# Performance work log

Measured on AMD Instinct MI355X. Metric: run time of the kernel, lower is better.

## Reference

```python
import jax, jax.numpy as jnp
import numpy as np

B, S, F, I, E, TOP_K, K, D, CLASSES = 2, 2048, 512, 1024, 8, 2, 7, 2, 8192
BETA = 0.9
INIT_SCALE = D ** -0.5


def setup_inputs() -> dict:
    key = jax.random.key(0)
    ks = jax.random.split(key, 10)
    s = lambda *shape: shape
    return {
        "inp": jax.random.randint(ks[0], (B, S), 0, CLASSES),
        "embed": jax.random.normal(ks[1], (CLASSES, 2 * F), jnp.float32) * 0.02,
        "gate_in_w": jax.random.normal(ks[2], (D, F, E), jnp.float32) * (F ** -0.5),
        "w_in": jax.random.normal(ks[3], (D, E, F, I), jnp.float32) * (F ** -0.5),
        "conv_w": jax.random.normal(ks[4], (D, I, I, K), jnp.float32) * ((I * K) ** -0.5),
        "gate_out_w": jax.random.normal(ks[5], (D, I, E), jnp.float32) * (I ** -0.5),
        "w_out": jax.random.normal(ks[6], (D, E, I, 3 * F), jnp.float32) * (I ** -0.5),
        "out_w": jax.random.normal(ks[7], (CLASSES, 2 * F), jnp.float32) * ((2 * F) ** -0.5),
        "out_b": jnp.zeros((CLASSES,), jnp.float32),
    }


def _moe(x, gate_w, expert_w):
    # x: [T, Fin]; NaiveGate top-k routing + grouped-GEMM combine.
    logits = x @ gate_w                                  # [T, E]
    top_vals, top_idx = jax.lax.top_k(logits, TOP_K)     # [T, k]
    scores = jax.nn.softmax(top_vals, axis=-1)           # softmax over selected experts
    n_exp = gate_w.shape[1]
    combine = jnp.sum(scores[:, :, None] * jax.nn.one_hot(top_idx, n_exp, dtype=x.dtype), axis=1)  # [T, E]
    y = jnp.einsum("tf,efo->teo", x, expert_w)           # dense all-expert eval
    return jnp.einsum("teo,te->to", y, combine)


def _norm(out):
    # custom norm over channel dim (dim 1 of [B, C, S])
    out = out - out.mean(axis=1, keepdims=True)
    c = out.shape[1]
    return out / (jnp.linalg.norm(out, axis=1, keepdims=True) * (c ** -0.5) + 1e-5)


def _cell(x, gate_in, win, cw, gate_out, wout, divisor):
    # x: [B, F, S]
    b, f, seq = x.shape
    t = x.transpose(0, 2, 1).reshape(b * seq, f)
    h = jax.nn.relu(_moe(t, gate_in, win))               # [T, I]
    h = h.reshape(b, seq, -1).transpose(0, 2, 1)         # [B, I, S]
    # causal depthwise-style conv (groups=1), left-pad K-1
    h = jax.lax.conv_general_dilated(h, cw, (1,), [(cw.shape[-1] - 1, 0)],
                                     dimension_numbers=("NCH", "OIH", "NCH"))
    h = jax.nn.relu(h)
    t2 = h.transpose(0, 2, 1).reshape(b * seq, -1)
    o = _moe(t2, gate_out, wout).reshape(b, seq, 3 * f).transpose(0, 2, 1)  # [B, 3F, S]
    depth_, scale, shift = jnp.split(o, 3, axis=1)
    cum = jnp.cumsum(depth_, axis=2)                      # running sum over sequence
    out = cum / divisor * scale + shift
    return _norm(out) * INIT_SCALE


def reference(inp, embed, gate_in_w, w_in, conv_w, gate_out_w, w_out, out_w, out_b):
    emb = embed[inp]                                      # [B, S, 2F]
    x = emb.transpose(0, 2, 1)                            # [B, 2F, S]
    x0, x1 = x[:, :F], x[:, F:]
    divisor = (jnp.arange(S, dtype=x.dtype) + 1.0)[None, None, :]
    for d in range(D):
        # momentum coupling with LinearAttentionCell
        f = _cell(x1, gate_in_w[d], w_in[d], conv_w[d], gate_out_w[d], w_out[d], divisor)
        y = x0 * BETA + f * (1.0 - BETA)
        x0, x1 = x1, y
        # additive coupling with Identity
        y = x0 + x1
        x0, x1 = x1, y
    out = jnp.concatenate([x0, x1], axis=1)               # [B, 2F, S]
    logits = jnp.einsum("bcs,kc->bks", out, out_w) + out_b[None, :, None]
    return logits
```

## Files before the change

### kernel.cpp

```cpp
#include <hip/hip_runtime.h>
#include <math.h>

typedef unsigned short u16;
typedef unsigned int   u32;

#define B_ 2
#define S_ 2048
#define F_ 512
#define I_ 1024
#define E_ 8
#define KW_ 7
#define D_ 2
#define CLASSES_ 8192
#define T_ (B_*S_)
#define SP_ (S_+6)
#define NSLOT_ 9216
#define GMAX_ 72

typedef __bf16 bf16x8 __attribute__((ext_vector_type(8)));
typedef float  f32x4  __attribute__((ext_vector_type(4)));

__device__ __forceinline__ u16 f2b(float f) {
    u32 x = __float_as_uint(f);
    return (u16)((x + 0x7fffu + ((x >> 16) & 1u)) >> 16);
}
__device__ __forceinline__ void fsplit(float v, u16& h, u16& l) {
    u16 hh = f2b(v);
    float hv = __uint_as_float(((u32)hh) << 16);
    h = hh;
    l = f2b(v - hv);
}

template<int N> __device__ __forceinline__ void waitvm() {
    asm volatile("s_waitcnt vmcnt(%0)" :: "n"(N) : "memory");
}

#define GLDS16(g, l) __builtin_amdgcn_global_load_lds( \
    (const __attribute__((address_space(1))) u32*)(g), \
    (__attribute__((address_space(3))) u32*)(l), 16, 0, 0)

__global__ void embed_k(const int* __restrict__ inp, const float* __restrict__ emb,
                        float* __restrict__ X0, float* __restrict__ X1,
                        int* __restrict__ stok, int* __restrict__ cnt)
{
    int t = blockIdx.x;
    int r = inp[t];
    const float* e = emb + (size_t)r * (2*F_);
    for (int c = threadIdx.x; c < F_; c += 256) {
        X0[(size_t)t*F_ + c] = e[c];
        X1[(size_t)t*F_ + c] = e[F_ + c];
    }
    int gi = blockIdx.x * 256 + threadIdx.x;
    if (gi < NSLOT_) stok[gi] = -1;
    if (gi < E_) cnt[gi] = 0;
}

template<int MODE, int W>
__global__ __launch_bounds__(512) void gatev_k(const float* __restrict__ X,
                                               const float* __restrict__ X2,
                                               const float* __restrict__ GW,
                                               int2* __restrict__ e2, float2* __restrict__ w2,
                                               int* __restrict__ cnt)
{
    __shared__ float gw[W*E_];
    for (int i = threadIdx.x; i < W*E_; i += 512) {
        int f = i >> 3, e = i & 7;
        gw[e*W + f] = GW[i];
    }
    __syncthreads();
    int wv = threadIdx.x >> 6, l = threadIdx.x & 63;
    int t = blockIdx.x * 8 + wv;
    const float* xr  = X + (size_t)t * W;
    const float* x2r = MODE ? (X2 + (size_t)t * W) : nullptr;
    float a[8];
    #pragma unroll
    for (int e = 0; e < 8; e++) a[e] = 0.f;
    #pragma unroll
    for (int c = 0; c < W/256; c++) {
        int f = c*256 + l*4;
        float4 x = *(const float4*)(xr + f);
        if (MODE) {
            float4 y = *(const float4*)(x2r + f);
            x.x = fmaxf(x.x + y.x, 0.f); x.y = fmaxf(x.y + y.y, 0.f);
            x.z = fmaxf(x.z + y.z, 0.f); x.w = fmaxf(x.w + y.w, 0.f);
        }
        #pragma unroll
        for (int e = 0; e < 8; e++) {
            float4 g = *(const float4*)(gw + e*W + f);
            a[e] += x.x*g.x + x.y*g.y + x.z*g.z + x.w*g.w;
        }
    }
    #pragma unroll
    for (int e = 0; e < 8; e++) {
        #pragma unroll
        for (int off = 32; off; off >>= 1) a[e] += __shfl_xor(a[e], off);
    }
    if (l == 0) {
        float v0 = -3.4e38f, v1 = -3.4e38f; int i0 = 0, i1 = 0;
        #pragma unroll
        for (int k = 0; k < E_; k++) {
            float v = a[k];
            if (v > v0)      { v1 = v0; i1 = i0; v0 = v; i0 = k; }
            else if (v > v1) { v1 = v;  i1 = k; }
        }
        float ex = expf(v1 - v0);
        e2[t] = make_int2(i0, i1);
        w2[t] = make_float2(1.f/(1.f+ex), ex/(1.f+ex));
        atomicAdd(&cnt[i0], 1);
        atomicAdd(&cnt[i1], 1);
    }
}

__global__ __launch_bounds__(256) void schedscat_k(const int* __restrict__ cnt,
                                                   const int2* __restrict__ e2,
                                                   const float2* __restrict__ w2,
                                                   int4* __restrict__ s0, int4* __restrict__ s1,
                                                   int split,
                                                   int* __restrict__ stok, float* __restrict__ sw)
{
    __shared__ int lpos[E_];
    int tid = threadIdx.x;
    int nb[E_], slotst[E_], gst[E_];
    int poff = 0, g0 = 0, g1 = 0;
    #pragma unroll
    for (int e = 0; e < E_; e++) {
        int n = (cnt[e] + 127) >> 7;
        nb[e] = n;
        slotst[e] = poff;
        if (e < split) { gst[e] = g0; g0 += n; }
        else           { gst[e] = g1; g1 += n; }
        poff += n << 7;
    }
    if (tid < E_) lpos[tid] = slotst[tid];
    if (tid < GMAX_) {
        int4 en = make_int4(0,0,0,0);
        for (int e = 0; e < split; e++)
            if (tid >= gst[e] && tid < gst[e] + nb[e])
                en = make_int4(slotst[e] + (tid - gst[e])*128, e, 1, 0);
        s0[tid] = en;
    }
    if (split < E_ && tid >= 128 && tid < 128 + GMAX_) {
        int j = tid - 128;
        int4 en = make_int4(0,0,0,0);
        for (int e = split; e < E_; e++)
            if (j >= gst[e] && j < gst[e] + nb[e])
                en = make_int4(slotst[e] + (j - gst[e])*128, e - split, 1, 0);
        s1[j] = en;
    }
    __syncthreads();
    for (int t = tid; t < T_; t += 256) {
        int2 e = e2[t]; float2 w = w2[t];
        int p0 = atomicAdd(&lpos[e.x], 1);
        stok[p0] = t;          sw[p0] = w.x;
        int p1 = atomicAdd(&lpos[e.y], 1);
        stok[p1] = t | 4096;   sw[p1] = w.y;
    }
}

__global__ __launch_bounds__(256) void transp_k(const float* __restrict__ src0,
                                                u16* __restrict__ dh, u16* __restrict__ dl,
                                                int R, int C)
{
    __shared__ float tl[32][33];
    int z = blockIdx.z;
    const float* src = src0 + (size_t)z * R * C;
    size_t dbase = (size_t)z * R * C;
    int c0 = blockIdx.x * 32, r0 = blockIdx.y * 32;
    int tx = threadIdx.x & 31, ty = threadIdx.x >> 5;
    #pragma unroll
    for (int j = 0; j < 32; j += 8)
        tl[ty + j][tx] = src[(size_t)(r0 + ty + j) * C + c0 + tx];
    __syncthreads();
    #pragma unroll
    for (int j = 0; j < 32; j += 8) {
        u16 h, l; fsplit(tl[tx][ty + j], h, l);
        size_t idx = dbase + (size_t)(c0 + ty + j) * R + r0 + tx;
        dh[idx] = h; dl[idx] = l;
    }
}

__global__ __launch_bounds__(256) void convw_k(const float* __restrict__ src,
                                               u16* __restrict__ dh, u16* __restrict__ dl)
{
    __shared__ float row[KW_*I_];
    int o = blockIdx.x;
    const float* s = src + (size_t)o * (KW_*I_);
    for (int c = threadIdx.x; c < KW_*I_; c += 256) row[c] = s[c];
    __syncthreads();
    size_t base = (size_t)o * (KW_*I_);
    for (int j = threadIdx.x; j < KW_*I_; j += 256) {
        int kc = j >> 10, i = j & 1023;
        u16 h, l; fsplit(row[i*KW_ + kc], h, l);
        dh[base + j] = h; dl[base + j] = l;
    }
}

__global__ void split_k(const float* __restrict__ src, u16* __restrict__ dh, u16* __restrict__ dl)
{
    size_t i = ((size_t)blockIdx.x * 256 + threadIdx.x) * 4;
    float4 v = *(const float4*)(src + i);
    ushort4 oh, ol;
    fsplit(v.x, oh.x, ol.x); fsplit(v.y, oh.y, ol.y);
    fsplit(v.z, oh.z, ol.z); fsplit(v.w, oh.w, ol.w);
    *(ushort4*)(dh + i) = oh;
    *(ushort4*)(dl + i) = ol;
}

__global__ void splith_k(const float* __restrict__ src, u16* __restrict__ dh)
{
    size_t i = ((size_t)blockIdx.x * 256 + threadIdx.x) * 4;
    float4 v = *(const float4*)(src + i);
    ushort4 oh;
    oh.x = f2b(v.x); oh.y = f2b(v.y); oh.z = f2b(v.z); oh.w = f2b(v.w);
    *(ushort4*)(dh + i) = oh;
}

__global__ void hsplit_k(const float* __restrict__ Ha, const float* __restrict__ Hb,
                         u16* __restrict__ ph, u16* __restrict__ pl)
{
    int gid = blockIdx.x*256 + threadIdx.x;
    int eb = gid * 4;
    int t = eb >> 10, c = eb & 1023;
    float4 a = *(const float4*)(Ha + eb);
    float4 b = *(const float4*)(Hb + eb);
    ushort4 hh, ll;
    fsplit(fmaxf(a.x+b.x,0.f), hh.x, ll.x); fsplit(fmaxf(a.y+b.y,0.f), hh.y, ll.y);
    fsplit(fmaxf(a.z+b.z,0.f), hh.z, ll.z); fsplit(fmaxf(a.w+b.w,0.f), hh.w, ll.w);
    size_t row = (size_t)(t >> 11)*SP_ + 6 + (t & (S_-1));
    *(ushort4*)(ph + (row << 10) + c) = hh;
    *(ushort4*)(pl + (row << 10) + c) = ll;
}

__global__ void crelu_k(const float* __restrict__ a0, const float* __restrict__ a1,
                        u16* __restrict__ dh, u16* __restrict__ dl,
                        int* __restrict__ stok, int* __restrict__ cnt)
{
    size_t i = ((size_t)blockIdx.x * 256 + threadIdx.x) * 4;
    float4 a = *(const float4*)(a0 + i);
    float4 b = *(const float4*)(a1 + i);
    ushort4 hh, ll;
    fsplit(fmaxf(a.x+b.x,0.f), hh.x, ll.x); fsplit(fmaxf(a.y+b.y,0.f), hh.y, ll.y);
    fsplit(fmaxf(a.z+b.z,0.f), hh.z, ll.z); fsplit(fmaxf(a.w+b.w,0.f), hh.w, ll.w);
    *(ushort4*)(dh + i) = hh;
    *(ushort4*)(dl + i) = ll;
    int gi = blockIdx.x * 256 + threadIdx.x;
    if (gi < NSLOT_) stok[gi] = -1;
    if (gi < E_) cnt[gi] = 0;
}

__global__ void hpadzero_k(u16* __restrict__ ph, u16* __restrict__ pl)
{
    int idx = blockIdx.x*256 + threadIdx.x;
    int b = idx / (6*I_);
    int rem = idx - b*(6*I_);
    size_t a = ((size_t)b*SP_ + (rem >> 10))*I_ + (rem & 1023);
    ph[a] = 0; pl[a] = 0;
}

enum { A_SPLIT=0, A_CONV=1, A_GATHER2=2 };
enum { EP_RANK=0, EP_DUAL=1, EP_FINAL=2 };

#define SBSZ(Pv) ((((Pv)==3)?16384:8192) + 8192*(((Pv)>=2)?2:1))

template<int AM, int EP, int PASSES, int SWZ, int PRIO>
__global__ __launch_bounds__(256, ((2*SBSZ(PASSES)) <= 32768) ? 4 : (((2*SBSZ(PASSES)) <= 49152) ? 3 : 2))
void mgemm(const void* __restrict__ A1, const void* __restrict__ A2,
           const u16* __restrict__ Bh, const u16* __restrict__ Bl,
           float* __restrict__ Ca, float* __restrict__ Cb,
           int N, int Kd, int ldb,
           const int4* __restrict__ sched, const int* __restrict__ stok,
           const float* __restrict__ sw, const float* __restrict__ bias)
{
    constexpr bool HAL = (PASSES==3);
    constexpr bool HBL = (PASSES>=2);
    constexpr int OAL  = 8192;
    constexpr int OBH  = (HAL ? 16384 : 8192);
    constexpr int OBL  = OBH + 8192;
    constexpr int SB   = OBH + 8192*(HBL ? 2 : 1);
    constexpr int NLOADS = 2*(HBL ? 2 : 1) + 2*(HAL ? 2 : 1);
    __shared__ uint4 ldsv[2*SB/16];
    char* lds = (char*)ldsv;

    const int tid  = threadIdx.x;
    const int lane = tid & 63, wid = tid >> 6;
    int n0 = blockIdx.x * 128;

    int slot0 = 0, m0 = 0, koff = 0, kz = 0;
    const u16 *bhb = Bh, *blb = Bl;
    if (AM == A_GATHER2) {
        int4 sc = sched[blockIdx.y];
        if (!sc.z) return;
        slot0 = sc.x;
        size_t wo = (size_t)sc.y * N * ldb;
        bhb = Bh + wo; blb = Bl + wo;
    } else if (AM == A_CONV) {
        if (SWZ == 1) {
            int fid = blockIdx.y * 8 + blockIdx.x;
            int xcd = fid & 7, k = fid >> 3;
            int mp = (xcd >> 1) * 8 + (k >> 3);
            int np = (xcd & 1) * 8 + (k & 7);
            m0 = mp * 128;
            kz = np >> 3;
            koff = kz * Kd;
            n0 = (np & 7) * 128;
        } else {
            m0 = (blockIdx.y & 31) * 128;
            kz = blockIdx.y >> 5;
            koff = kz * Kd;
        }
    } else {
        m0 = blockIdx.y * 128;
    }

    int srow[2], klog[2];
    #pragma unroll
    for (int c = 0; c < 2; c++) {
        int row = (tid >> 2) + c*64;
        srow[c] = row;
        klog[c] = ((tid & 3) ^ ((row >> 1) & 3)) << 3;
    }

    const u16 *bgh[2], *bgl[2];
    #pragma unroll
    for (int c = 0; c < 2; c++) {
        size_t off = (size_t)(n0 + srow[c]) * ldb + koff + klog[c];
        bgh[c] = bhb + off;
        bgl[c] = blb + off;
    }

    const u16 *a1p[2], *a2p[2];
    #pragma unroll
    for (int c = 0; c < 2; c++) {
        if (AM == A_SPLIT) {
            size_t off = (size_t)(m0 + srow[c]) * Kd + klog[c];
            a1p[c] = (const u16*)A1 + off;
            a2p[c] = (const u16*)A2 + off;
        } else if (AM == A_CONV) {
            int t = m0 + srow[c];
            size_t rb = (((size_t)(t >> 11)*SP_ + (t & (S_-1))) << 10) + koff + klog[c];
            a1p[c] = (const u16*)A1 + rb;
            a2p[c] = (const u16*)A2 + rb;
        } else {
            int s = stok[slot0 + srow[c]];
            int tk = (s < 0) ? 0 : (s & 4095);
            size_t off = (size_t)tk * Kd + klog[c];
            a1p[c] = (const u16*)A1 + off;
            a2p[c] = (const u16*)A2 + off;
        }
    }

    const int wr = wid >> 1, wc = wid & 1;
    const int l15 = lane & 15, kq = lane >> 4;
    int aoff[4], boff[4];
    #pragma unroll
    for (int m = 0; m < 4; m++) {
        int ra = wr*64 + m*16 + l15;
        aoff[m] = ra*64 + ((kq ^ ((ra >> 1) & 3)) << 4);
    }
    #pragma unroll
    for (int n = 0; n < 4; n++) {
        int rb = wc*64 + n*16 + l15;
        boff[n] = rb*64 + ((kq ^ ((rb >> 1) & 3)) << 4);
    }

    f32x4 acc[4][4];
    #pragma unroll
    for (int m = 0; m < 4; m++)
        #pragma unroll
        for (int n = 0; n < 4; n++) acc[m][n] = {0.f,0.f,0.f,0.f};

    const int nt = Kd >> 5;

#define STAGE_GL(K0, BB)                                                          \
    {                                                                             \
        _Pragma("unroll")                                                         \
        for (int c = 0; c < 2; c++) {                                             \
            GLDS16(bgh[c] + (K0), lds + (BB) + OBH + c*4096 + (wid<<10));         \
            if (HBL)                                                              \
                GLDS16(bgl[c] + (K0), lds + (BB) + OBL + c*4096 + (wid<<10));     \
        }                                                                         \
        _Pragma("unroll")                                                         \
        for (int c = 0; c < 2; c++) {                                             \
            GLDS16(a1p[c] + (K0), lds + (BB) + c*4096 + (wid<<10));               \
            if (HAL)                                                              \
                GLDS16(a2p[c] + (K0), lds + (BB) + OAL + c*4096 + (wid<<10));     \
        }                                                                         \
    }

    STAGE_GL(0, 0);
    STAGE_GL(32, SB);
    waitvm<NLOADS>();
    __builtin_amdgcn_s_barrier();

    for (int it = 0; it < nt; ++it) {
        const int bb = (it & 1) * SB;
        {
            bf16x8 ah[4], al[4], bhf[4], blf[4];
            #pragma unroll
            for (int m = 0; m < 4; m++) {
                ah[m] = *(const bf16x8*)(lds + bb + aoff[m]);
                if (HAL) al[m] = *(const bf16x8*)(lds + bb + OAL + aoff[m]);
            }
            #pragma unroll
            for (int n = 0; n < 4; n++) {
                bhf[n] = *(const bf16x8*)(lds + bb + OBH + boff[n]);
                if (HBL) blf[n] = *(const bf16x8*)(lds + bb + OBL + boff[n]);
            }
            if (PRIO) __builtin_amdgcn_s_setprio(1);
            #pragma unroll
            for (int m = 0; m < 4; m++)
                #pragma unroll
                for (int n = 0; n < 4; n++) {
                    acc[m][n] = __builtin_amdgcn_mfma_f32_16x16x32_bf16(ah[m], bhf[n], acc[m][n], 0, 0, 0);
                    if (HAL)
                        acc[m][n] = __builtin_amdgcn_mfma_f32_16x16x32_bf16(al[m], bhf[n], acc[m][n], 0, 0, 0);
                    if (HBL)
                        acc[m][n] = __builtin_amdgcn_mfma_f32_16x16x32_bf16(ah[m], blf[n], acc[m][n], 0, 0, 0);
                }
            if (PRIO) __builtin_amdgcn_s_setprio(0);
        }
        asm volatile("s_waitcnt lgkmcnt(0)" ::: "memory");
        __builtin_amdgcn_sched_barrier(0);
        __builtin_amdgcn_s_barrier();
        if (it + 2 < nt) {
            STAGE_GL((it + 2) << 5, bb);
            waitvm<NLOADS>();
            __builtin_amdgcn_s_barrier();
        } else if (it + 1 < nt) {
            waitvm<0>();
            __builtin_amdgcn_s_barrier();
        }
    }

    #pragma unroll
    for (int m = 0; m < 4; m++) {
        #pragma unroll
        for (int n = 0; n < 4; n++) {
            f32x4 v = acc[m][n];
            int rl0 = wr*64 + m*16 + (lane >> 4)*4;
            int col = n0 + wc*64 + n*16 + l15;
            #pragma unroll
            for (int j = 0; j < 4; j++) {
                float x = v[j];
                int rl = rl0 + j;
                if (EP == EP_RANK) {
                    int s = stok[slot0 + rl];
                    if (s >= 0) {
                        int tt = s & 4095;
                        float ww = sw[slot0 + rl];
                        float* dst = (s & 4096) ? Cb : Ca;
                        dst[(size_t)tt * N + col] = ww * x;
                    }
                } else if (EP == EP_DUAL) {
                    int r = m0 + rl;
                    float* dst = kz ? Cb : Ca;
                    dst[(size_t)r * N + col] = x;
                } else {
                    int r = m0 + rl;
                    x += bias[r];
                    int b = col >> 11, s = col & (S_-1);
                    Ca[(((size_t)(b*CLASSES_ + r)) << 11) + s] = x;
                }
            }
        }
    }
#undef STAGE_GL
}

#define SC_ 128
#define NCH_ (S_/SC_)
__global__ void cum1(const float* __restrict__ Oa, const float* __restrict__ Ob,
                     float* __restrict__ CS)
{
    int blk = blockIdx.x;
    int b = blk / NCH_, ch = blk % NCH_;
    int c = threadIdx.x;
    int s0 = ch * SC_;
    size_t base = ((size_t)(b*S_ + s0)) * (3*F_) + c;
    float sum = 0.f;
    for (int s = 0; s < SC_; s++) {
        size_t idx = base + (size_t)s * (3*F_);
        sum += Oa[idx] + Ob[idx];
    }
    CS[(size_t)blk * F_ + c] = sum;
}
__global__ void cum23(const float* __restrict__ Oa, const float* __restrict__ Ob,
                      const float* __restrict__ CS, float* __restrict__ FP)
{
    int blk = blockIdx.x;
    int b = blk / NCH_, ch = blk % NCH_;
    int c = threadIdx.x;
    float run = 0.f;
    for (int j = 0; j < ch; j++) run += CS[(size_t)(b*NCH_ + j) * F_ + c];
    int s0 = ch * SC_;
    for (int s = s0; s < s0 + SC_; s++) {
        size_t t = (size_t)b * S_ + s;
        size_t ro = t * (3*F_);
        run += Oa[ro + c] + Ob[ro + c];
        float scl = Oa[ro + F_ + c] + Ob[ro + F_ + c];
        float shf = Oa[ro + 2*F_ + c] + Ob[ro + 2*F_ + c];
        FP[t*F_ + c] = run / (float)(s + 1) * scl + shf;
    }
}

__global__ __launch_bounds__(256) void normupd_k(const float* __restrict__ FP,
                                                 float* __restrict__ X0, float* __restrict__ X1,
                                                 u16* __restrict__ xch,
                                                 int* __restrict__ stok, int* __restrict__ cnt)
{
    __shared__ float sb[4];
    int t = blockIdx.x;
    const float* row = FP + (size_t)t * F_;
    int tid = threadIdx.x;
    float v0 = row[tid], v1 = row[tid + 256];
    float s = v0 + v1;
    #pragma unroll
    for (int off = 32; off; off >>= 1) s += __shfl_xor(s, off);
    int w = tid >> 6;
    if ((tid & 63) == 0) sb[w] = s;
    __syncthreads();
    float mean = (sb[0] + sb[1] + sb[2] + sb[3]) * (1.0f / F_);
    v0 -= mean; v1 -= mean;
    float q = v0*v0 + v1*v1;
    #pragma unroll
    for (int off = 32; off; off >>= 1) q += __shfl_xor(q, off);
    __syncthreads();
    if ((tid & 63) == 0) sb[w] = q;
    __syncthreads();
    float ss = sb[0] + sb[1] + sb[2] + sb[3];
    float denom = sqrtf(ss) * 0.04419417382415922f + 1e-5f;
    float sc = 0.70710678118654752f / denom;
    float f0 = v0 * sc, f1 = v1 * sc;
    size_t i0 = (size_t)t * F_ + tid, i1 = i0 + 256;
    float a0 = 0.9f * X0[i0] + 0.1f * f0;
    float a1 = 0.9f * X0[i1] + 0.1f * f1;
    float x1n0 = X1[i0] + a0;
    float x1n1 = X1[i1] + a1;
    X0[i0] = a0; X1[i0] = x1n0;
    X0[i1] = a1; X1[i1] = x1n1;
    if (xch) {
        size_t xb = (size_t)t * (2*F_);
        xch[xb + tid]            = f2b(a0);
        xch[xb + tid + 256]      = f2b(a1);
        xch[xb + F_ + tid]       = f2b(x1n0);
        xch[xb + F_ + tid + 256] = f2b(x1n1);
    }
    int gi = blockIdx.x * 256 + tid;
    if (gi < NSLOT_) stok[gi] = -1;
    if (gi < E_) cnt[gi] = 0;
}

extern "C" void kernel_launch(void* const* d_in, const int* in_sizes, int n_in,
                              void* d_out, int out_size, void* d_ws, size_t ws_size,
                              hipStream_t stream)
{
    const int*   inp    = (const int*)  d_in[0];
    const float* embed  = (const float*)d_in[1];
    const float* gin_w  = (const float*)d_in[2];
    const float* w_in   = (const float*)d_in[3];
    const float* conv_w = (const float*)d_in[4];
    const float* gout_w = (const float*)d_in[5];
    const float* w_out  = (const float*)d_in[6];
    const float* out_w  = (const float*)d_in[7];
    const float* out_b  = (const float*)d_in[8];
    float* out = (float*)d_out;

    char* w = (char*)d_ws;
    auto alloc = [&](size_t bytes) { char* r = w; w += (bytes + 255) & ~(size_t)255; return r; };
    float* X0    = (float*)alloc((size_t)T_*F_*4);
    float* X1    = (float*)alloc((size_t)T_*F_*4);
    u16*   Hpadh = (u16*)  alloc((size_t)B_*SP_*I_*2);
    u16*   Hpadl = (u16*)  alloc((size_t)B_*SP_*I_*2);
    u16*   HCh   = (u16*)  alloc((size_t)T_*I_*2);
    u16*   HCl   = (u16*)  alloc((size_t)T_*I_*2);
    float* FP    = (float*)alloc((size_t)T_*F_*4);
    float* CS    = (float*)alloc((size_t)B_*NCH_*F_*4);
    char*  ar1   = alloc((size_t)T_*3*F_*4);
    char*  ar2   = alloc((size_t)T_*I_*4);
    char*  altr  = alloc((size_t)T_*3*F_*4);
    u16*   Wh    = (u16*)  alloc((size_t)I_*KW_*I_*2);
    u16*   Wl    = (u16*)  alloc((size_t)I_*KW_*I_*2);
    int2*  e2    = (int2*) alloc((size_t)T_*8);
    float2* w2   = (float2*)alloc((size_t)T_*8);
    int*   stok  = (int*)  alloc((size_t)NSLOT_*4);
    float* sw    = (float*)alloc((size_t)NSLOT_*4);
    int*   cnt   = (int*)  alloc(64);
    int4*  s0    = (int4*) alloc((size_t)GMAX_*16);
    int4*  s1    = (int4*) alloc((size_t)GMAX_*16);

    float* Ha  = (float*)ar1;
    float* Oa  = (float*)ar1;
    float* HC0 = (float*)ar2;
    float* Hb  = (float*)altr;
    float* HC1 = (float*)altr;
    float* Ob  = (float*)altr;
    u16*   X1h = (u16*)FP;
    u16*   X1l = X1h + (size_t)T_*F_;
    u16*   Xch = (u16*)ar1;
    u16*   OWh = (u16*)ar2;

    embed_k<<<T_, 256, 0, stream>>>(inp, embed, X0, X1, stok, cnt);
    hpadzero_k<<<(B_*6*I_)/256, 256, 0, stream>>>(Hpadh, Hpadl);

    for (int d = 0; d < D_; ++d) {
        gatev_k<0, F_><<<T_/8, 512, 0, stream>>>(X1, nullptr, gin_w + (size_t)d*F_*E_, e2, w2, cnt);
        schedscat_k<<<1, 256, 0, stream>>>(cnt, e2, w2, s0, s1, 8, stok, sw);
        split_k<<<(T_*F_)/1024, 256, 0, stream>>>(X1, X1h, X1l);
        transp_k<<<dim3(I_/32, F_/32, E_), 256, 0, stream>>>(
            w_in + (size_t)d*E_*F_*I_, Wh, Wl, F_, I_);
        mgemm<A_GATHER2, EP_RANK, 3, 0, 0><<<dim3(I_/128, GMAX_), 256, 0, stream>>>(
            X1h, X1l, Wh, Wl, Ha, Hb, I_, F_, F_, s0, stok, sw, nullptr);
        hsplit_k<<<T_*I_/1024, 256, 0, stream>>>(Ha, Hb, Hpadh, Hpadl);

        convw_k<<<I_, 256, 0, stream>>>(conv_w + (size_t)d*I_*I_*KW_, Wh, Wl);
        mgemm<A_CONV, EP_DUAL, 3, 1, 1><<<dim3(8, 64), 256, 0, stream>>>(
            Hpadh, Hpadl, Wh, Wl, HC0, HC1, I_, (KW_*I_)/2, KW_*I_, nullptr, nullptr, nullptr, nullptr);
        crelu_k<<<T_*I_/1024, 256, 0, stream>>>(HC0, HC1, HCh, HCl, stok, cnt);

        gatev_k<1, I_><<<T_/8, 512, 0, stream>>>(HC0, HC1, gout_w + (size_t)d*I_*E_, e2, w2, cnt);
        schedscat_k<<<1, 256, 0, stream>>>(cnt, e2, w2, s0, s1, 4, stok, sw);
        for (int c = 0; c < 2; ++c) {
            transp_k<<<dim3((3*F_)/32, I_/32, 4), 256, 0, stream>>>(
                w_out + (size_t)d*E_*I_*(3*F_) + (size_t)c*4*I_*(3*F_), Wh, Wl, I_, 3*F_);
            const int4* sc = (c == 0) ? s0 : s1;
            if (d == 0)
                mgemm<A_GATHER2, EP_RANK, 3, 0, 0><<<dim3((3*F_)/128, GMAX_), 256, 0, stream>>>(
                    HCh, HCl, Wh, Wl, Oa, Ob, 3*F_, I_, I_, sc, stok, sw, nullptr);
            else
                mgemm<A_GATHER2, EP_RANK, 1, 0, 0><<<dim3((3*F_)/128, GMAX_), 256, 0, stream>>>(
                    HCh, HCl, Wh, Wl, Oa, Ob, 3*F_, I_, I_, sc, stok, sw, nullptr);
        }

        cum1<<<B_*NCH_, F_, 0, stream>>>(Oa, Ob, CS);
        cum23<<<B_*NCH_, F_, 0, stream>>>(Oa, Ob, CS, FP);
        normupd_k<<<T_, 256, 0, stream>>>(FP, X0, X1,
                                          (d == D_-1) ? Xch : (u16*)nullptr, stok, cnt);
    }

    splith_k<<<(CLASSES_*2*F_)/1024, 256, 0, stream>>>(out_w, OWh);
    mgemm<A_SPLIT, EP_FINAL, 1, 0, 0><<<dim3(T_/128, CLASSES_/128), 256, 0, stream>>>(
        OWh, OWh, Xch, Xch, out, nullptr, T_, 2*F_, 2*F_, nullptr, nullptr, nullptr, out_b);
}
```

Measured before the change: 1.416 ms.

## Store X1 as bf16 hi/lo split and fuse crelu into output gate

```diff
diff --git a/kernel.cpp b/kernel.cpp
--- a/kernel.cpp
+++ b/kernel.cpp
@@ -24,6 +24,9 @@
     u32 x = __float_as_uint(f);
     return (u16)((x + 0x7fffu + ((x >> 16) & 1u)) >> 16);
 }
+__device__ __forceinline__ float b2f(u16 h) {
+    return __uint_as_float(((u32)h) << 16);
+}
 __device__ __forceinline__ void fsplit(float v, u16& h, u16& l) {
     u16 hh = f2b(v);
     float hv = __uint_as_float(((u32)hh) << 16);
@@ -40,7 +43,7 @@
     (__attribute__((address_space(3))) u32*)(l), 16, 0, 0)
 
 __global__ void embed_k(const int* __restrict__ inp, const float* __restrict__ emb,
-                        float* __restrict__ X0, float* __restrict__ X1,
+                        float* __restrict__ X0, u16* __restrict__ X1h, u16* __restrict__ X1l,
                         int* __restrict__ stok, int* __restrict__ cnt)
 {
     int t = blockIdx.x;
@@ -48,45 +51,104 @@
     const float* e = emb + (size_t)r * (2*F_);
     for (int c = threadIdx.x; c < F_; c += 256) {
         X0[(size_t)t*F_ + c] = e[c];
-        X1[(size_t)t*F_ + c] = e[F_ + c];
+        u16 h, l; fsplit(e[F_ + c], h, l);
+        X1h[(size_t)t*F_ + c] = h;
+        X1l[(size_t)t*F_ + c] = l;
     }
     int gi = blockIdx.x * 256 + threadIdx.x;
     if (gi < NSLOT_) stok[gi] = -1;
     if (gi < E_) cnt[gi] = 0;
 }
 
-template<int MODE, int W>
-__global__ __launch_bounds__(512) void gatev_k(const float* __restrict__ X,
-                                               const float* __restrict__ X2,
-                                               const float* __restrict__ GW,
-                                               int2* __restrict__ e2, float2* __restrict__ w2,
-                                               int* __restrict__ cnt)
-{
-    __shared__ float gw[W*E_];
-    for (int i = threadIdx.x; i < W*E_; i += 512) {
+__global__ __launch_bounds__(512) void gatebf_k(const u16* __restrict__ Xh,
+                                                const u16* __restrict__ Xl,
+                                                const float* __restrict__ GW,
+                                                int2* __restrict__ e2, float2* __restrict__ w2,
+                                                int* __restrict__ cnt)
+{
+    __shared__ float gw[F_*E_];
+    for (int i = threadIdx.x; i < F_*E_; i += 512) {
         int f = i >> 3, e = i & 7;
-        gw[e*W + f] = GW[i];
+        gw[e*F_ + f] = GW[i];
     }
     __syncthreads();
     int wv = threadIdx.x >> 6, l = threadIdx.x & 63;
     int t = blockIdx.x * 8 + wv;
-    const float* xr  = X + (size_t)t * W;
-    const float* x2r = MODE ? (X2 + (size_t)t * W) : nullptr;
+    const u16* xh = Xh + (size_t)t * F_;
+    const u16* xl = Xl + (size_t)t * F_;
     float a[8];
     #pragma unroll
     for (int e = 0; e < 8; e++) a[e] = 0.f;
     #pragma unroll
-    for (int c = 0; c < W/256; c++) {
+    for (int c = 0; c < F_/256; c++) {
+        int f = c*256 + l*4;
+        ushort4 h4 = *(const ushort4*)(xh + f);
+        ushort4 l4 = *(const ushort4*)(xl + f);
+        float4 x;
+        x.x = b2f(h4.x) + b2f(l4.x); x.y = b2f(h4.y) + b2f(l4.y);
+        x.z = b2f(h4.z) + b2f(l4.z); x.w = b2f(h4.w) + b2f(l4.w);
+        #pragma unroll
+        for (int e = 0; e < 8; e++) {
+            float4 g = *(const float4*)(gw + e*F_ + f);
+            a[e] += x.x*g.x + x.y*g.y + x.z*g.z + x.w*g.w;
+        }
+    }
+    #pragma unroll
+    for (int e = 0; e < 8; e++) {
+        #pragma unroll
+        for (int off = 32; off; off >>= 1) a[e] += __shfl_xor(a[e], off);
+    }
+    if (l == 0) {
+        float v0 = -3.4e38f, v1 = -3.4e38f; int i0 = 0, i1 = 0;
+        #pragma unroll
+        for (int k = 0; k < E_; k++) {
+            float v = a[k];
+            if (v > v0)      { v1 = v0; i1 = i0; v0 = v; i0 = k; }
+            else if (v > v1) { v1 = v;  i1 = k; }
+        }
+        float ex = expf(v1 - v0);
+        e2[t] = make_int2(i0, i1);
+        w2[t] = make_float2(1.f/(1.f+ex), ex/(1.f+ex));
+        atomicAdd(&cnt[i0], 1);
+        atomicAdd(&cnt[i1], 1);
+    }
+}
+
+__global__ __launch_bounds__(512) void gatecrelu_k(const float* __restrict__ A0,
+                                                   const float* __restrict__ A1v,
+                                                   const float* __restrict__ GW,
+                                                   u16* __restrict__ Hh, u16* __restrict__ Hl,
+                                                   int2* __restrict__ e2, float2* __restrict__ w2,
+                                                   int* __restrict__ cnt)
+{
+    __shared__ float gw[I_*E_];
+    for (int i = threadIdx.x; i < I_*E_; i += 512) {
+        int f = i >> 3, e = i & 7;
+        gw[e*I_ + f] = GW[i];
+    }
+    __syncthreads();
+    int wv = threadIdx.x >> 6, l = threadIdx.x & 63;
+    int t = blockIdx.x * 8 + wv;
+    const float* xr  = A0 + (size_t)t * I_;
+    const float* x2r = A1v + (size_t)t * I_;
+    float a[8];
+    #pragma unroll
+    for (int e = 0; e < 8; e++) a[e] = 0.f;
+    #pragma unroll
+    for (int c = 0; c < I_/256; c++) {
         int f = c*256 + l*4;
         float4 x = *(const float4*)(xr + f);
-        if (MODE) {
-            float4 y = *(const float4*)(x2r + f);
-            x.x = fmaxf(x.x + y.x, 0.f); x.y = fmaxf(x.y + y.y, 0.f);
-            x.z = fmaxf(x.z + y.z, 0.f); x.w = fmaxf(x.w + y.w, 0.f);
-        }
+        float4 y = *(const float4*)(x2r + f);
+        x.x = fmaxf(x.x + y.x, 0.f); x.y = fmaxf(x.y + y.y, 0.f);
+        x.z = fmaxf(x.z + y.z, 0.f); x.w = fmaxf(x.w + y.w, 0.f);
+        ushort4 oh, ol;
+        fsplit(x.x, oh.x, ol.x); fsplit(x.y, oh.y, ol.y);
+        fsplit(x.z, oh.z, ol.z); fsplit(x.w, oh.w, ol.w);
+        *(ushort4*)(Hh + (size_t)t*I_ + f) = oh;
+        *(ushort4*)(Hl + (size_t)t*I_ + f) = ol;
         #pragma unroll
         for (int e = 0; e < 8; e++) {
-            float4 g = *(const float4*)(gw + e*W + f);
+            float4 g = *(const float4*)(gw + e*I_ + f);
             a[e] += x.x*g.x + x.y*g.y + x.z*g.z + x.w*g.w;
         }
     }
@@ -195,17 +257,6 @@
     }
 }
 
-__global__ void split_k(const float* __restrict__ src, u16* __restrict__ dh, u16* __restrict__ dl)
-{
-    size_t i = ((size_t)blockIdx.x * 256 + threadIdx.x) * 4;
-    float4 v = *(const float4*)(src + i);
-    ushort4 oh, ol;
-    fsplit(v.x, oh.x, ol.x); fsplit(v.y, oh.y, ol.y);
-    fsplit(v.z, oh.z, ol.z); fsplit(v.w, oh.w, ol.w);
-    *(ushort4*)(dh + i) = oh;
-    *(ushort4*)(dl + i) = ol;
-}
-
 __global__ void splith_k(const float* __restrict__ src, u16* __restrict__ dh)
 {
     size_t i = ((size_t)blockIdx.x * 256 + threadIdx.x) * 4;
@@ -216,7 +267,8 @@
 }
 
 __global__ void hsplit_k(const float* __restrict__ Ha, const float* __restrict__ Hb,
-                         u16* __restrict__ ph, u16* __restrict__ pl)
+                         u16* __restrict__ ph, u16* __restrict__ pl,
+                         int* __restrict__ stok, int* __restrict__ cnt)
 {
     int gid = blockIdx.x*256 + threadIdx.x;
     int eb = gid * 4;
@@ -229,23 +281,8 @@
     size_t row = (size_t)(t >> 11)*SP_ + 6 + (t & (S_-1));
     *(ushort4*)(ph + (row << 10) + c) = hh;
     *(ushort4*)(pl + (row << 10) + c) = ll;
-}
-
-__global__ void crelu_k(const float* __restrict__ a0, const float* __restrict__ a1,
-                        u16* __restrict__ dh, u16* __restrict__ dl,
-                        int* __restrict__ stok, int* __restrict__ cnt)
-{
-    size_t i = ((size_t)blockIdx.x * 256 + threadIdx.x) * 4;
-    float4 a = *(const float4*)(a0 + i);
-    float4 b = *(const float4*)(a1 + i);
-    ushort4 hh, ll;
-    fsplit(fmaxf(a.x+b.x,0.f), hh.x, ll.x); fsplit(fmaxf(a.y+b.y,0.f), hh.y, ll.y);
-    fsplit(fmaxf(a.z+b.z,0.f), hh.z, ll.z); fsplit(fmaxf(a.w+b.w,0.f), hh.w, ll.w);
-    *(ushort4*)(dh + i) = hh;
-    *(ushort4*)(dl + i) = ll;
-    int gi = blockIdx.x * 256 + threadIdx.x;
-    if (gi < NSLOT_) stok[gi] = -1;
-    if (gi < E_) cnt[gi] = 0;
+    if (gid < NSLOT_) stok[gid] = -1;
+    if (gid < E_) cnt[gid] = 0;
 }
 
 __global__ void hpadzero_k(u16* __restrict__ ph, u16* __restrict__ pl)
@@ -504,7 +541,8 @@
 }
 
 __global__ __launch_bounds__(256) void normupd_k(const float* __restrict__ FP,
-                                                 float* __restrict__ X0, float* __restrict__ X1,
+                                                 float* __restrict__ X0,
+                                                 u16* __restrict__ X1h, u16* __restrict__ X1l,
                                                  u16* __restrict__ xch,
                                                  int* __restrict__ stok, int* __restrict__ cnt)
 {
@@ -534,10 +572,14 @@
     size_t i0 = (size_t)t * F_ + tid, i1 = i0 + 256;
     float a0 = 0.9f * X0[i0] + 0.1f * f0;
     float a1 = 0.9f * X0[i1] + 0.1f * f1;
-    float x1n0 = X1[i0] + a0;
-    float x1n1 = X1[i1] + a1;
-    X0[i0] = a0; X1[i0] = x1n0;
-    X0[i1] = a1; X1[i1] = x1n1;
+    float x1o0 = b2f(X1h[i0]) + b2f(X1l[i0]);
+    float x1o1 = b2f(X1h[i1]) + b2f(X1l[i1]);
+    float x1n0 = x1o0 + a0;
+    float x1n1 = x1o1 + a1;
+    X0[i0] = a0; X0[i1] = a1;
+    u16 h, l;
+    fsplit(x1n0, h, l); X1h[i0] = h; X1l[i0] = l;
+    fsplit(x1n1, h, l); X1h[i1] = h; X1l[i1] = l;
     if (xch) {
         size_t xb = (size_t)t * (2*F_);
         xch[xb + tid]            = f2b(a0);
@@ -568,7 +610,8 @@
     char* w = (char*)d_ws;
     auto alloc = [&](size_t bytes) { char* r = w; w += (bytes + 255) & ~(size_t)255; return r; };
     float* X0    = (float*)alloc((size_t)T_*F_*4);
-    float* X1    = (float*)alloc((size_t)T_*F_*4);
+    u16*   X1h   = (u16*)  alloc((size_t)T_*F_*2);
+    u16*   X1l   = (u16*)  alloc((size_t)T_*F_*2);
     u16*   Hpadh = (u16*)  alloc((size_t)B_*SP_*I_*2);
     u16*   Hpadl = (u16*)  alloc((size_t)B_*SP_*I_*2);
     u16*   HCh   = (u16*)  alloc((size_t)T_*I_*2);
@@ -594,30 +637,27 @@
     float* Hb  = (float*)altr;
     float* HC1 = (float*)altr;
     float* Ob  = (float*)altr;
-    u16*   X1h = (u16*)FP;
-    u16*   X1l = X1h + (size_t)T_*F_;
     u16*   Xch = (u16*)ar1;
     u16*   OWh = (u16*)ar2;
 
-    embed_k<<<T_, 256, 0, stream>>>(inp, embed, X0, X1, stok, cnt);
+    embed_k<<<T_, 256, 0, stream>>>(inp, embed, X0, X1h, X1l, stok, cnt);
     hpadzero_k<<<(B_*6*I_)/256, 256, 0, stream>>>(Hpadh, Hpadl);
 
     for (int d = 0; d < D_; ++d) {
-        gatev_k<0, F_><<<T_/8, 512, 0, stream>>>(X1, nullptr, gin_w + (size_t)d*F_*E_, e2, w2, cnt);
+        gatebf_k<<<T_/8, 512, 0, stream>>>(X1h, X1l, gin_w + (size_t)d*F_*E_, e2, w2, cnt);
         schedscat_k<<<1, 256, 0, stream>>>(cnt, e2, w2, s0, s1, 8, stok, sw);
-        split_k<<<(T_*F_)/1024, 256, 0, stream>>>(X1, X1h, X1l);
         transp_k<<<dim3(I_/32, F_/32, E_), 256, 0, stream>>>(
             w_in + (size_t)d*E_*F_*I_, Wh, Wl, F_, I_);
         mgemm<A_GATHER2, EP_RANK, 3, 0, 0><<<dim3(I_/128, GMAX_), 256, 0, stream>>>(
             X1h, X1l, Wh, Wl, Ha, Hb, I_, F_, F_, s0, stok, sw, nullptr);
-        hsplit_k<<<T_*I_/1024, 256, 0, stream>>>(Ha, Hb, Hpadh, Hpadl);
+        hsplit_k<<<T_*I_/1024, 256, 0, stream>>>(Ha, Hb, Hpadh, Hpadl, stok, cnt);
 
         convw_k<<<I_, 256, 0, stream>>>(conv_w + (size_t)d*I_*I_*KW_, Wh, Wl);
         mgemm<A_CONV, EP_DUAL, 3, 1, 1><<<dim3(8, 64), 256, 0, stream>>>(
             Hpadh, Hpadl, Wh, Wl, HC0, HC1, I_, (KW_*I_)/2, KW_*I_, nullptr, nullptr, nullptr, nullptr);
-        crelu_k<<<T_*I_/1024, 256, 0, stream>>>(HC0, HC1, HCh, HCl, stok, cnt);
-
-        gatev_k<1, I_><<<T_/8, 512, 0, stream>>>(HC0, HC1, gout_w + (size_t)d*I_*E_, e2, w2, cnt);
+
+        gatecrelu_k<<<T_/8, 512, 0, stream>>>(HC0, HC1, gout_w + (size_t)d*I_*E_,
+                                              HCh, HCl, e2, w2, cnt);
         schedscat_k<<<1, 256, 0, stream>>>(cnt, e2, w2, s0, s1, 4, stok, sw);
         for (int c = 0; c < 2; ++c) {
             transp_k<<<dim3((3*F_)/32, I_/32, 4), 256, 0, stream>>>(
@@ -633,7 +673,7 @@
 
         cum1<<<B_*NCH_, F_, 0, stream>>>(Oa, Ob, CS);
         cum23<<<B_*NCH_, F_, 0, stream>>>(Oa, Ob, CS, FP);
-        normupd_k<<<T_, 256, 0, stream>>>(FP, X0, X1,
+        normupd_k<<<T_, 256, 0, stream>>>(FP, X0, X1h, X1l,
                                           (d == D_-1) ? Xch : (u16*)nullptr, stok, cnt);
     }
 
```

Measured after the change: 1.393 ms (median of 2 runs). No clear change (-1.6%).
